# Optimization experiments

Hardware: AMD Instinct MI355X
Metric: run time of the kernel (lower is better)

## Reference

```python
import jax, jax.numpy as jnp
import numpy as np

IN_SHAPE, OUT_SHAPE = 64, 256  # FoldingBlock(64, 256, ...)
REPEAT = OUT_SHAPE // IN_SHAPE  # 4


def sample_2d(m, n):
    # Reproduces SANet.points + SANet.sample_2D exactly (numpy constants).
    xs = np.linspace(-0.3, 0.3, 46)
    ys = np.linspace(-0.3, 0.3, 46)
    X, Y = np.meshgrid(xs, ys)            # (46,46) each, 'xy' indexing
    pts = np.stack([X, Y])                # (2,46,46)
    ix = np.round(np.linspace(0, 45, m)).astype(int)
    iy = np.round(np.linspace(0, 45, n)).astype(int)
    gx, gy = np.meshgrid(ix, iy)          # (n,m)
    p = pts[:, gx.ravel(), gy.ravel()].T  # (m*n, 2)
    return jnp.asarray(p, dtype=jnp.float32)


def _lin_relu(x, W, b):
    return jax.nn.relu(x @ W + b)


def setup_inputs() -> dict:
    key = jax.random.key(0)
    ks = jax.random.split(key, 16)
    s = 0.02  # small init scale keeps softmax logits well-conditioned
    d = {
        "p": jax.random.normal(ks[0], (128, 64, 512), dtype=jnp.float32),
        # upmlp1: MLP([514, 512]) (shared by both up() calls)
        "W_up": jax.random.normal(ks[1], (514, 512), dtype=jnp.float32) * s,
        "b_up": jnp.zeros((512,), jnp.float32),
        # self_attn1: M_h = MLP([1024,256])
        "Wh": jax.random.normal(ks[2], (1024, 256), dtype=jnp.float32) * s,
        "bh": jnp.zeros((256,), jnp.float32),
        # M_l = MLP([1024,256])
        "Wl": jax.random.normal(ks[3], (1024, 256), dtype=jnp.float32) * s,
        "bl": jnp.zeros((256,), jnp.float32),
        # M_g = MLP([1024,1024])
        "Wg": jax.random.normal(ks[4], (1024, 1024), dtype=jnp.float32) * s,
        "bg": jnp.zeros((1024,), jnp.float32),
        # M_f = MLP([1024,512,256]) -> two Linear+ReLU layers
        "Wf1": jax.random.normal(ks[5], (1024, 512), dtype=jnp.float32) * s,
        "bf1": jnp.zeros((512,), jnp.float32),
        "Wf2": jax.random.normal(ks[6], (512, 256), dtype=jnp.float32) * s,
        "bf2": jnp.zeros((256,), jnp.float32),
        # M_down: MLP([1024, 512])
        "W_down": jax.random.normal(ks[7], (1024, 512), dtype=jnp.float32) * s,
        "b_down": jnp.zeros((512,), jnp.float32),
        "m": 16,
        "n": 16,
    }
    return d


def _up(p, pts, W_up, b_up, Wh, bh, Wl, bl, Wg, bg, Wf1, bf1, Wf2, bf2):
    # p: (B, 64, 512) -> (B, 256, 512) via torch-style repeat (tile)
    B = p.shape[0]
    p = jnp.tile(p, (1, REPEAT, 1))
    p2d = jnp.concatenate([p, jnp.broadcast_to(pts[None], (B,) + pts.shape)], -1)  # (B,256,514)
    p2d = _lin_relu(p2d, W_up, b_up)                  # (B,256,512)
    p = jnp.concatenate([p, p2d], -1)                  # (B,256,1024)
    # SelfAttention (hand-rolled: separate projections + softmax + bmm)
    h = _lin_relu(p, Wh, bh)                           # (B,256,256)
    l = _lin_relu(p, Wl, bl)                           # (B,256,256)
    g = _lin_relu(p, Wg, bg)                           # (B,256,1024)
    mm = jnp.einsum("bmc,bnc->bmn", l, h)             # l @ h^T
    attn = jax.nn.softmax(mm, axis=-1)
    applied = jnp.einsum("bmn,bnc->bmc", attn, g)      # (B,256,1024)
    x = p + applied
    # M_f = MLP([1024,512,256]): ReLU after every Linear
    return _lin_relu(_lin_relu(x, Wf1, bf1), Wf2, bf2)  # (B,256,256)


def _down(p, W_down, b_down):
    # (B,256,256) -> (B,64,1024) -> MLP([1024,512])
    B = p.shape[0]
    p = p.reshape(B, IN_SHAPE, REPEAT * p.shape[2])
    return _lin_relu(p, W_down, b_down)                # (B,64,512)


def reference(p, W_up, b_up, Wh, bh, Wl, bl, Wg, bg, Wf1, bf1, Wf2, bf2,
              W_down, b_down, m, n):
    pts = sample_2d(int(m), int(n))                    # (m*n, 2) constant grid
    attn_params = (Wh, bh, Wl, bl, Wg, bg, Wf1, bf1, Wf2, bf2)
    p1 = _up(p, pts, W_up, b_up, *attn_params)         # (B,256,256)
    p2 = _down(p1, W_down, b_down)                     # (B,64,512)
    p_delta = p - p2
    p2u = _up(p_delta, pts, W_up, b_up, *attn_params)  # shared weights with first up
    return p1 + p2u                                    # (B,256,256)
```

## Files before the change

kernel.cpp:

```cpp
#include <hip/hip_runtime.h>
#include <cstdint>
#include <cstddef>


typedef unsigned short u16;
typedef __bf16 bf16x8 __attribute__((ext_vector_type(8)));
typedef float f32x4 __attribute__((ext_vector_type(4)));

__device__ __forceinline__ u16 f2bf(float f) {
    unsigned u = __builtin_bit_cast(unsigned, f);
    unsigned r = (u + 0x7fffu + ((u >> 16) & 1u)) >> 16;
    return (u16)r;
}
__device__ __forceinline__ float bf2f(u16 h) {
    unsigned u = ((unsigned)h) << 16;
    return __builtin_bit_cast(float, u);
}
__device__ __forceinline__ bf16x8 ldfrag(const u16* p) {
    return __builtin_bit_cast(bf16x8, *reinterpret_cast<const uint4*>(p));
}
__device__ __forceinline__ void gload16(const u16* g, u16* l) {
    __builtin_amdgcn_global_load_lds((__attribute__((address_space(1))) void*)g,
                                     (__attribute__((address_space(3))) void*)l,
                                     16, 0, 0);
}

template<bool BIG, int MODE>
__global__ __launch_bounds__(BIG ? 512 : 256, 2)
void mg(const u16* __restrict__ A0, const u16* __restrict__ A1,
        const u16* __restrict__ Bt, const float* __restrict__ bias,
        const float* __restrict__ EXf,
        float* __restrict__ outF, u16* __restrict__ outB,
        u16* __restrict__ out1, u16* __restrict__ out2,
        int K, long sB)
{
    constexpr int BM = BIG ? 256 : 128;
    constexpr int BN = BIG ? 256 : 128;
    constexpr int BK = BIG ? 32 : 64;
    constexpr int THREADS = BIG ? 512 : 256;
    constexpr int WN = BIG ? 4 : 2;
    constexpr int MI = BIG ? 8 : 4;
    constexpr int NJ = 4;
    constexpr int KS = BK / 32;
    constexpr int UPR = BK / 8;
    constexpr int UMASK = UPR - 1;
    constexpr int USH = BIG ? 2 : 3;
    constexpr int RA = (BM * UPR) / THREADS;
    constexpr int RB = (BN * UPR) / THREADS;

    __shared__ __align__(16) u16 As[2][BM * BK];
    __shared__ __align__(16) u16 Bs[2][BN * BK];

    const int b    = blockIdx.z;
    const int tid  = threadIdx.x;
    const int lane = tid & 63;
    const int w    = tid >> 6;
    const int wr   = w / WN, wc = w % WN;
    const int wrow0 = wr * (BM / (THREADS / 64 / WN));
    const int wcol0 = wc * (BN / WN);
    const int gm0  = blockIdx.y * BM;
    const int gn0  = blockIdx.x * BN;
    const int lm   = lane & 15, hk = lane >> 4;

    const int NT = K / BK;

    auto stage = [&](int kt, int buf) {
        const int kb = kt * BK;
        #pragma unroll
        for (int t = 0; t < RA; ++t) {
            const int idx = tid + t * THREADS;
            const int row = idx >> USH, u = idx & UMASK;
            const int kk = kb + ((u ^ (row & UMASK)) << 3);
            const u16* ga;
            if constexpr (MODE == 0) {
                ga = A0 + ((size_t)b << 15) + (size_t)((gm0 + row) & 63) * 512 + kk;
            } else if constexpr (MODE == 1) {
                const int gr = gm0 + row;
                ga = (kk < 512) ? A0 + ((size_t)b << 15) + (size_t)(gr & 63) * 512 + kk
                                : A1 + ((size_t)b << 17) + (size_t)gr * 512 + (kk - 512);
            } else if constexpr (MODE == 2 || MODE == 3) {
                ga = A0 + ((size_t)b << 16) + (size_t)(gm0 + row) * 256 + kk;
            } else if constexpr (MODE == 4) {
                ga = A0 + ((size_t)b << 18) + (size_t)(gm0 + row) * 1024 + kk;
            } else if constexpr (MODE == 5) {
                ga = A0 + ((size_t)b << 17) + (size_t)(gm0 + row) * 512 + kk;
            } else {
                int gr = gm0 + row; if (gr > 63) gr = 63;
                ga = A0 + ((size_t)b << 16) + (size_t)(gr * 4 + (kk >> 8)) * 256 + (kk & 255);
            }
            gload16(ga, &As[buf][(size_t)(w * 64 + t * THREADS) * 8]);
        }
        #pragma unroll
        for (int t = 0; t < RB; ++t) {
            const int idx = tid + t * THREADS;
            const int row = idx >> USH, u = idx & UMASK;
            const int kk = kb + ((u ^ (row & UMASK)) << 3);
            gload16(Bt + (size_t)b * sB + (size_t)(gn0 + row) * K + kk,
                    &Bs[buf][(size_t)(w * 64 + t * THREADS) * 8]);
        }
    };

    f32x4 acc[MI][NJ];
    #pragma unroll
    for (int i = 0; i < MI; ++i)
        #pragma unroll
        for (int j = 0; j < NJ; ++j)
            acc[i][j] = (f32x4){0.f, 0.f, 0.f, 0.f};

    stage(0, 0);
    stage(1, 1);

    for (int kt = 0; kt < NT; ++kt) {
        const int cur = kt & 1;
        if (kt == NT - 1) {
            asm volatile("s_waitcnt vmcnt(0)" ::: "memory");
        } else if constexpr (RA + RB == 4) {
            asm volatile("s_waitcnt vmcnt(4)" ::: "memory");
        } else {
            asm volatile("s_waitcnt vmcnt(8)" ::: "memory");
        }
        __builtin_amdgcn_s_barrier();
        asm volatile("" ::: "memory");

        #pragma unroll
        for (int ks = 0; ks < KS; ++ks) {
            bf16x8 af[MI], bfr[NJ];
            #pragma unroll
            for (int i = 0; i < MI; ++i) {
                const int row = wrow0 + i * 16 + lm;
                af[i] = ldfrag(&As[cur][(size_t)row * BK + (((ks * 4 + hk) ^ (row & UMASK)) << 3)]);
            }
            #pragma unroll
            for (int j = 0; j < NJ; ++j) {
                const int row = wcol0 + j * 16 + lm;
                bfr[j] = ldfrag(&Bs[cur][(size_t)row * BK + (((ks * 4 + hk) ^ (row & UMASK)) << 3)]);
            }
            __builtin_amdgcn_s_setprio(1);
            #pragma unroll
            for (int i = 0; i < MI; ++i)
                #pragma unroll
                for (int j = 0; j < NJ; ++j)
                    acc[i][j] = __builtin_amdgcn_mfma_f32_16x16x32_bf16(af[i], bfr[j], acc[i][j], 0, 0, 0);
            __builtin_amdgcn_s_setprio(0);
        }

        asm volatile("" ::: "memory");
        __builtin_amdgcn_s_barrier();
        if (kt + 2 < NT) stage(kt + 2, cur);
    }

    #pragma unroll
    for (int i = 0; i < MI; ++i) {
        #pragma unroll
        for (int r = 0; r < 4; ++r) {
            const int row = gm0 + wrow0 + i * 16 + hk * 4 + r;
            if (MODE == 6 && row >= 64) continue;
            #pragma unroll
            for (int j = 0; j < NJ; ++j) {
                const int col = gn0 + wcol0 + j * 16 + lm;
                float v = acc[i][j][r];
                if constexpr (MODE == 0) {
                    const float px = -0.3f + 0.04f * (float)(row >> 4);
                    const float py = -0.3f + 0.04f * (float)(row & 15);
                    v += px * EXf[(size_t)512 * 512 + col] + py * EXf[(size_t)513 * 512 + col];
                    v = fmaxf(v + bias[col], 0.0f);
                    outB[((size_t)b << 17) + (size_t)row * 512 + col] = f2bf(v);
                } else if constexpr (MODE == 1) {
                    v = fmaxf(v + bias[col], 0.0f);
                    if (col < 256)      outB[((size_t)b << 16) + (size_t)row * 256 + col] = f2bf(v);
                    else if (col < 512) out1[((size_t)b << 16) + (size_t)row * 256 + (col - 256)] = f2bf(v);
                    else                out2[((size_t)b << 18) + (size_t)row * 1024 + (col - 512)] = f2bf(v);
                } else if constexpr (MODE == 2) {
                    outF[((size_t)b << 16) + (size_t)row * 256 + col] = v;
                } else if constexpr (MODE == 3) {
                    float cv = (col < 512)
                        ? EXf[((size_t)b << 15) + (size_t)(row & 63) * 512 + col]
                        : bf2f(A1[((size_t)b << 17) + (size_t)row * 512 + (col - 512)]);
                    v += cv;
                    outB[((size_t)b << 18) + (size_t)row * 1024 + col] = f2bf(v);
                } else if constexpr (MODE == 4) {
                    v = fmaxf(v + bias[col], 0.0f);
                    outB[((size_t)b << 17) + (size_t)row * 512 + col] = f2bf(v);
                } else if constexpr (MODE == 5) {
                    v = fmaxf(v + bias[col], 0.0f);
                    const size_t oidx = ((size_t)b << 16) + (size_t)row * 256 + col;
                    if (EXf) v += EXf[oidx];
                    outF[oidx] = v;
                    if (outB) outB[oidx] = f2bf(v);
                } else if constexpr (MODE == 6) {
                    v = fmaxf(v + bias[col], 0.0f);
                    const size_t oidx = ((size_t)b << 15) + (size_t)row * 512 + col;
                    v = EXf[oidx] - v;
                    outF[oidx] = v;
                    outB[oidx] = f2bf(v);
                }
            }
        }
    }
}

template<bool F32IN>
__global__ __launch_bounds__(256)
void transpose_k(const void* __restrict__ in_, u16* __restrict__ out, int R, int C)
{
    __shared__ float t[64][65];
    const size_t zo = (size_t)blockIdx.z * (size_t)R * C;
    const int c0 = blockIdx.x * 64, r0 = blockIdx.y * 64;
    const int x = threadIdx.x, y = threadIdx.y;
    #pragma unroll
    for (int i = 0; i < 16; ++i) {
        const int r = y * 16 + i;
        float v;
        if constexpr (F32IN) v = ((const float*)in_)[zo + (size_t)(r0 + r) * C + c0 + x];
        else                 v = bf2f(((const u16*)in_)[zo + (size_t)(r0 + r) * C + c0 + x]);
        t[r][x] = v;
    }
    __syncthreads();
    #pragma unroll
    for (int i = 0; i < 16; ++i) {
        const int c = y * 16 + i;
        out[zo + (size_t)(c0 + c) * R + r0 + x] = f2bf(t[x][c]);
    }
}

__global__ __launch_bounds__(256)
void cvt_k(const float* __restrict__ in, u16* __restrict__ out, int n4)
{
    int i = blockIdx.x * 256 + threadIdx.x;
    const int stride = gridDim.x * 256;
    for (; i < n4; i += stride) {
        float4 v = ((const float4*)in)[i];
        ushort4 o;
        o.x = f2bf(v.x); o.y = f2bf(v.y); o.z = f2bf(v.z); o.w = f2bf(v.w);
        ((ushort4*)out)[i] = o;
    }
}

__global__ __launch_bounds__(512)
void concat3_k(const float* __restrict__ a, const float* __restrict__ bb,
               const float* __restrict__ c, float* __restrict__ o)
{
    const int i = blockIdx.x * 512 + threadIdx.x;
    if (i < 256)       o[i] = a[i];
    else if (i < 512)  o[i] = bb[i - 256];
    else if (i < 1536) o[i] = c[i - 512];
}

__global__ __launch_bounds__(64)
void softmax_k(const float* __restrict__ logits, u16* __restrict__ attn)
{
    const size_t row = blockIdx.x;
    const float4 v = ((const float4*)(logits + row * 256))[threadIdx.x];
    float mx = fmaxf(fmaxf(v.x, v.y), fmaxf(v.z, v.w));
    #pragma unroll
    for (int o = 32; o > 0; o >>= 1) mx = fmaxf(mx, __shfl_xor(mx, o));
    float e0 = expf(v.x - mx), e1 = expf(v.y - mx), e2 = expf(v.z - mx), e3 = expf(v.w - mx);
    float s = e0 + e1 + e2 + e3;
    #pragma unroll
    for (int o = 32; o > 0; o >>= 1) s += __shfl_xor(s, o);
    const float inv = 1.0f / s;
    ushort4 o;
    o.x = f2bf(e0 * inv); o.y = f2bf(e1 * inv); o.z = f2bf(e2 * inv); o.w = f2bf(e3 * inv);
    ((ushort4*)(attn + row * 256))[threadIdx.x] = o;
}

extern "C" void kernel_launch(void* const* d_in, const int* in_sizes, int n_in,
                              void* d_out, int out_size, void* d_ws, size_t ws_size,
                              hipStream_t stream)
{
    const float* p      = (const float*)d_in[0];
    const float* W_up   = (const float*)d_in[1];
    const float* b_up   = (const float*)d_in[2];
    const float* Wh     = (const float*)d_in[3];
    const float* bh     = (const float*)d_in[4];
    const float* Wl     = (const float*)d_in[5];
    const float* bl     = (const float*)d_in[6];
    const float* Wg     = (const float*)d_in[7];
    const float* bg     = (const float*)d_in[8];
    const float* Wf1    = (const float*)d_in[9];
    const float* bf1    = (const float*)d_in[10];
    const float* Wf2    = (const float*)d_in[11];
    const float* bf2v   = (const float*)d_in[12];
    const float* W_down = (const float*)d_in[13];
    const float* b_down = (const float*)d_in[14];

    const int B = in_sizes[0] / 32768;
    float* out = (float*)d_out;

    char* wsp = (char*)d_ws;
    auto alloc = [&](size_t bytes) -> char* {
        char* r = wsp; wsp += (bytes + 255) & ~(size_t)255; return r;
    };

    u16* WupT  = (u16*)alloc((size_t)512 * 512 * 2);
    u16* WhlgT = (u16*)alloc((size_t)1536 * 1024 * 2);
    u16* Wf1T  = (u16*)alloc((size_t)512 * 1024 * 2);
    u16* Wf2T  = (u16*)alloc((size_t)256 * 512 * 2);
    u16* WdT   = (u16*)alloc((size_t)512 * 1024 * 2);
    float* bias_hlg = (float*)alloc((size_t)1536 * 4);
    u16* pbf   = (u16*)alloc((size_t)B * 32768 * 2);

    const size_t fixed_used = (size_t)(wsp - (char*)d_ws);
    const size_t perB = 2555904;
    int BC = B;
    while (BC > 1 && fixed_used + (size_t)BC * perB > ws_size) BC >>= 1;

    u16* upout = (u16*)alloc((size_t)BC * 131072 * 2);
    u16* gb    = (u16*)alloc((size_t)BC * 262144 * 2);
    u16* gT    = (u16*)alloc((size_t)BC * 262144 * 2);
    u16* xb    = gb;
    u16* hb    = (u16*)alloc((size_t)BC * 65536 * 2);
    u16* lb    = (u16*)alloc((size_t)BC * 65536 * 2);
    u16* atb   = (u16*)alloc((size_t)BC * 65536 * 2);
    u16* p1bf  = (u16*)alloc((size_t)BC * 65536 * 2);
    u16* pdbf  = (u16*)alloc((size_t)BC * 32768 * 2);
    float* lgt = (float*)alloc((size_t)BC * 65536 * 4);
    float* p1f = (float*)alloc((size_t)BC * 65536 * 4);
    float* pdf = (float*)alloc((size_t)BC * 32768 * 4);

    const dim3 tb(64, 4);
    {
        int n4 = B * 8192;
        int nb = (n4 + 255) / 256; if (nb > 2048) nb = 2048;
        cvt_k<<<dim3(nb), dim3(256), 0, stream>>>(p, pbf, n4);
        transpose_k<true><<<dim3(8, 8, 1),  tb, 0, stream>>>(W_up, WupT, 512, 512);
        transpose_k<true><<<dim3(4, 16, 1), tb, 0, stream>>>(Wh, WhlgT, 1024, 256);
        transpose_k<true><<<dim3(4, 16, 1), tb, 0, stream>>>(Wl, WhlgT + (size_t)256 * 1024, 1024, 256);
        transpose_k<true><<<dim3(16, 16, 1),tb, 0, stream>>>(Wg, WhlgT + (size_t)512 * 1024, 1024, 1024);
        transpose_k<true><<<dim3(8, 16, 1), tb, 0, stream>>>(Wf1, Wf1T, 1024, 512);
        transpose_k<true><<<dim3(4, 8, 1),  tb, 0, stream>>>(Wf2, Wf2T, 512, 256);
        transpose_k<true><<<dim3(8, 16, 1), tb, 0, stream>>>(W_down, WdT, 1024, 512);
        concat3_k<<<dim3(3), dim3(512), 0, stream>>>(bh, bl, bg, bias_hlg);
    }

    auto run_up = [&](const u16* pin_bf, const float* pin_f32,
                      float* f2outF, u16* f2outB, const float* f2EXf, int bc) {
        mg<false,0><<<dim3(4, 2, bc), dim3(256), 0, stream>>>(
            pin_bf, nullptr, WupT, b_up, W_up, nullptr, upout, nullptr, nullptr, 512, 0);
        mg<true,1><<<dim3(6, 1, bc), dim3(512), 0, stream>>>(
            pin_bf, upout, WhlgT, bias_hlg, nullptr, nullptr, hb, lb, gb, 1024, 0);
        mg<false,2><<<dim3(2, 2, bc), dim3(256), 0, stream>>>(
            lb, nullptr, hb, nullptr, nullptr, lgt, nullptr, nullptr, nullptr, 256, 65536);
        softmax_k<<<dim3(bc * 256), dim3(64), 0, stream>>>(lgt, atb);
        transpose_k<false><<<dim3(16, 4, bc), tb, 0, stream>>>(gb, gT, 256, 1024);
        mg<true,3><<<dim3(4, 1, bc), dim3(512), 0, stream>>>(
            atb, upout, gT, nullptr, pin_f32, nullptr, xb, nullptr, nullptr, 256, 262144);
        mg<false,4><<<dim3(4, 2, bc), dim3(256), 0, stream>>>(
            xb, nullptr, Wf1T, bf1, nullptr, nullptr, upout, nullptr, nullptr, 1024, 0);
        mg<false,5><<<dim3(2, 2, bc), dim3(256), 0, stream>>>(
            upout, nullptr, Wf2T, bf2v, f2EXf, f2outF, f2outB, nullptr, nullptr, 512, 0);
    };

    for (int b0 = 0; b0 < B; b0 += BC) {
        const int bc = (B - b0 < BC) ? (B - b0) : BC;
        const u16*   pin_bf  = pbf + (size_t)b0 * 32768;
        const float* pin_f32 = p   + (size_t)b0 * 32768;
        run_up(pin_bf, pin_f32, p1f, p1bf, nullptr, bc);
        mg<false,6><<<dim3(4, 1, bc), dim3(256), 0, stream>>>(
            p1bf, nullptr, WdT, b_down, pin_f32, pdf, pdbf, nullptr, nullptr, 1024, 0);
        run_up(pdbf, pdf, out + (size_t)b0 * 65536, nullptr, p1f, bc);
    }
}
```

Measured before the change: 1.023 ms.

## Split GEMM kernel into 256-tile 4-stage pipelined variant and fuse g transpose

Adds a dedicated 512-thread 256x256-tile GEMM kernel with a four-slot LDS ring (prefetch three tiles ahead, issued before the MFMAs) and a k-major unswizzled LDS layout. It is used for the up, hlg, attention-apply and f1 stages, while the small-tile kernel stays for logits, f2 and down. The hlg kernel now writes the g output already transposed, which removes the separate transpose launch. The down stage no longer writes an fp32 delta, and the second up pass reads the bf16 delta instead. The logits buffer is aliased onto xb to shrink the workspace, at the cost of 128KB LDS per block, which lowers occupancy, and of some precision in the residual.

```diff
diff --git a/kernel.cpp b/kernel.cpp
--- a/kernel.cpp
+++ b/kernel.cpp
@@ -25,121 +25,255 @@
                                      16, 0, 0);
 }
 
-template<bool BIG, int MODE>
-__global__ __launch_bounds__(BIG ? 512 : 256, 2)
-void mg(const u16* __restrict__ A0, const u16* __restrict__ A1,
+template<int MODE>
+__global__ __launch_bounds__(512, 2)
+void bg(const u16* __restrict__ A0, const u16* __restrict__ A1,
         const u16* __restrict__ Bt, const float* __restrict__ bias,
-        const float* __restrict__ EXf,
-        float* __restrict__ outF, u16* __restrict__ outB,
-        u16* __restrict__ out1, u16* __restrict__ out2,
+        const float* __restrict__ EXf, const u16* __restrict__ EXb,
+        u16* __restrict__ outB, u16* __restrict__ out1, u16* __restrict__ out2,
         int K, long sB)
 {
-    constexpr int BM = BIG ? 256 : 128;
-    constexpr int BN = BIG ? 256 : 128;
-    constexpr int BK = BIG ? 32 : 64;
-    constexpr int THREADS = BIG ? 512 : 256;
-    constexpr int WN = BIG ? 4 : 2;
-    constexpr int MI = BIG ? 8 : 4;
-    constexpr int NJ = 4;
-    constexpr int KS = BK / 32;
-    constexpr int UPR = BK / 8;
-    constexpr int UMASK = UPR - 1;
-    constexpr int USH = BIG ? 2 : 3;
-    constexpr int RA = (BM * UPR) / THREADS;
-    constexpr int RB = (BN * UPR) / THREADS;
-
-    __shared__ __align__(16) u16 As[2][BM * BK];
-    __shared__ __align__(16) u16 Bs[2][BN * BK];
+    __shared__ __align__(16) u16 As[4][256 * 32];
+    __shared__ __align__(16) u16 Bs[4][256 * 32];
 
     const int b    = blockIdx.z;
     const int tid  = threadIdx.x;
     const int lane = tid & 63;
     const int w    = tid >> 6;
-    const int wr   = w / WN, wc = w % WN;
-    const int wrow0 = wr * (BM / (THREADS / 64 / WN));
-    const int wcol0 = wc * (BN / WN);
-    const int gm0  = blockIdx.y * BM;
-    const int gn0  = blockIdx.x * BN;
+    const int wr   = w >> 2;
+    const int wc   = w & 3;
+    const int wrow0 = wr * 128;
+    const int wcol0 = wc * 64;
+    const int gn0  = blockIdx.x * 256;
     const int lm   = lane & 15, hk = lane >> 4;
 
+    const int NT = K / 32;
+
+    auto stage = [&](int kt, int slot) {
+        const int kb = kt * 32;
+        #pragma unroll
+        for (int t = 0; t < 2; ++t) {
+            const int idx = tid + t * 512;
+            const int U   = idx >> 8;
+            const int row = idx & 255;
+            const int k   = kb + U * 8;
+            const u16* ga;
+            if constexpr (MODE == 0) {
+                ga = A0 + ((size_t)b << 15) + (size_t)(row & 63) * 512 + k;
+            } else if constexpr (MODE == 1) {
+                ga = (k < 512) ? A0 + ((size_t)b << 15) + (size_t)(row & 63) * 512 + k
+                               : A1 + ((size_t)b << 17) + (size_t)row * 512 + (k - 512);
+            } else if constexpr (MODE == 3) {
+                ga = A0 + ((size_t)b << 16) + (size_t)row * 256 + k;
+            } else {
+                ga = A0 + ((size_t)b << 18) + (size_t)row * 1024 + k;
+            }
+            gload16(ga, &As[slot][(size_t)(t * 512 + w * 64) * 8]);
+        }
+        #pragma unroll
+        for (int t = 0; t < 2; ++t) {
+            const int idx = tid + t * 512;
+            const int U   = idx >> 8;
+            const int row = idx & 255;
+            const int k   = kb + U * 8;
+            gload16(Bt + (size_t)b * sB + (size_t)(gn0 + row) * K + k,
+                    &Bs[slot][(size_t)(t * 512 + w * 64) * 8]);
+        }
+    };
+
+    f32x4 acc[8][4];
+    #pragma unroll
+    for (int i = 0; i < 8; ++i)
+        #pragma unroll
+        for (int j = 0; j < 4; ++j)
+            acc[i][j] = (f32x4){0.f, 0.f, 0.f, 0.f};
+
+    stage(0, 0);
+    stage(1, 1);
+    stage(2, 2);
+
+    for (int kt = 0; kt < NT; ++kt) {
+        const int s = kt & 3;
+        const int rem = NT - 1 - kt;
+        if (rem >= 2)      asm volatile("s_waitcnt vmcnt(8)" ::: "memory");
+        else if (rem == 1) asm volatile("s_waitcnt vmcnt(4)" ::: "memory");
+        else               asm volatile("s_waitcnt vmcnt(0)" ::: "memory");
+        __builtin_amdgcn_s_barrier();
+        asm volatile("" ::: "memory");
+
+        bf16x8 af[8], bfr[4];
+        #pragma unroll
+        for (int i = 0; i < 8; ++i)
+            af[i] = ldfrag(&As[s][(size_t)hk * 2048 + (size_t)(wrow0 + i * 16 + lm) * 8]);
+        #pragma unroll
+        for (int j = 0; j < 4; ++j)
+            bfr[j] = ldfrag(&Bs[s][(size_t)hk * 2048 + (size_t)(wcol0 + j * 16 + lm) * 8]);
+
+        if (kt + 3 < NT) stage(kt + 3, (kt + 3) & 3);
+
+        __builtin_amdgcn_s_setprio(1);
+        #pragma unroll
+        for (int i = 0; i < 8; ++i)
+            #pragma unroll
+            for (int j = 0; j < 4; ++j)
+                acc[i][j] = __builtin_amdgcn_mfma_f32_16x16x32_bf16(af[i], bfr[j], acc[i][j], 0, 0, 0);
+        __builtin_amdgcn_s_setprio(0);
+        asm volatile("" ::: "memory");
+    }
+
+    #pragma unroll
+    for (int i = 0; i < 8; ++i) {
+        const int rowb = wrow0 + i * 16 + hk * 4;
+        #pragma unroll
+        for (int j = 0; j < 4; ++j) {
+            const int col = gn0 + wcol0 + j * 16 + lm;
+            float v4[4];
+            #pragma unroll
+            for (int r = 0; r < 4; ++r) v4[r] = acc[i][j][r];
+
+            if constexpr (MODE == 0) {
+                #pragma unroll
+                for (int r = 0; r < 4; ++r) {
+                    const int row = rowb + r;
+                    float v = v4[r];
+                    const float px = -0.3f + 0.04f * (float)(row >> 4);
+                    const float py = -0.3f + 0.04f * (float)(row & 15);
+                    v += px * EXf[(size_t)512 * 512 + col] + py * EXf[(size_t)513 * 512 + col];
+                    v = fmaxf(v + bias[col], 0.0f);
+                    outB[((size_t)b << 17) + (size_t)row * 512 + col] = f2bf(v);
+                }
+            } else if constexpr (MODE == 1) {
+                if (col < 512) {
+                    #pragma unroll
+                    for (int r = 0; r < 4; ++r) {
+                        const int row = rowb + r;
+                        float v = fmaxf(v4[r] + bias[col], 0.0f);
+                        if (col < 256) outB[((size_t)b << 16) + (size_t)row * 256 + col] = f2bf(v);
+                        else           out1[((size_t)b << 16) + (size_t)row * 256 + (col - 256)] = f2bf(v);
+                    }
+                } else {
+                    ushort4 o;
+                    o.x = f2bf(fmaxf(v4[0] + bias[col], 0.0f));
+                    o.y = f2bf(fmaxf(v4[1] + bias[col], 0.0f));
+                    o.z = f2bf(fmaxf(v4[2] + bias[col], 0.0f));
+                    o.w = f2bf(fmaxf(v4[3] + bias[col], 0.0f));
+                    *reinterpret_cast<ushort4*>(out2 + ((size_t)b << 18) +
+                        (size_t)(col - 512) * 256 + rowb) = o;
+                }
+            } else if constexpr (MODE == 3) {
+                #pragma unroll
+                for (int r = 0; r < 4; ++r) {
+                    const int row = rowb + r;
+                    float v = v4[r];
+                    float cv;
+                    if (col < 512) {
+                        const size_t ridx = ((size_t)b << 15) + (size_t)(row & 63) * 512 + col;
+                        cv = EXf ? EXf[ridx] : bf2f(EXb[ridx]);
+                    } else {
+                        cv = bf2f(A1[((size_t)b << 17) + (size_t)row * 512 + (col - 512)]);
+                    }
+                    v += cv;
+                    outB[((size_t)b << 18) + (size_t)row * 1024 + col] = f2bf(v);
+                }
+            } else {
+                #pragma unroll
+                for (int r = 0; r < 4; ++r) {
+                    const int row = rowb + r;
+                    float v = fmaxf(v4[r] + bias[col], 0.0f);
+                    outB[((size_t)b << 17) + (size_t)row * 512 + col] = f2bf(v);
+                }
+            }
+        }
+    }
+}
+
+template<int MODE>
+__global__ __launch_bounds__(256, 2)
+void mg(const u16* __restrict__ A0, const u16* __restrict__ Bt,
+        const float* __restrict__ bias, const float* __restrict__ EXf,
+        float* __restrict__ outF, u16* __restrict__ outB,
+        int K, long sB)
+{
+    constexpr int BK = 64;
+    constexpr int UMASK = 7;
+
+    __shared__ __align__(16) u16 As[2][128 * 64];
+    __shared__ __align__(16) u16 Bs[2][128 * 64];
+
+    const int b    = blockIdx.z;
+    const int tid  = threadIdx.x;
+    const int lane = tid & 63;
+    const int w    = tid >> 6;
+    const int wr   = w >> 1, wc = w & 1;
+    const int wrow0 = wr * 64, wcol0 = wc * 64;
+    const int gm0  = blockIdx.y * 128;
+    const int gn0  = blockIdx.x * 128;
+    const int lm   = lane & 15, hk = lane >> 4;
     const int NT = K / BK;
 
     auto stage = [&](int kt, int buf) {
         const int kb = kt * BK;
         #pragma unroll
-        for (int t = 0; t < RA; ++t) {
-            const int idx = tid + t * THREADS;
-            const int row = idx >> USH, u = idx & UMASK;
+        for (int t = 0; t < 4; ++t) {
+            const int idx = tid + t * 256;
+            const int row = idx >> 3, u = idx & UMASK;
             const int kk = kb + ((u ^ (row & UMASK)) << 3);
             const u16* ga;
-            if constexpr (MODE == 0) {
-                ga = A0 + ((size_t)b << 15) + (size_t)((gm0 + row) & 63) * 512 + kk;
-            } else if constexpr (MODE == 1) {
-                const int gr = gm0 + row;
-                ga = (kk < 512) ? A0 + ((size_t)b << 15) + (size_t)(gr & 63) * 512 + kk
-                                : A1 + ((size_t)b << 17) + (size_t)gr * 512 + (kk - 512);
-            } else if constexpr (MODE == 2 || MODE == 3) {
+            if constexpr (MODE == 2) {
                 ga = A0 + ((size_t)b << 16) + (size_t)(gm0 + row) * 256 + kk;
-            } else if constexpr (MODE == 4) {
-                ga = A0 + ((size_t)b << 18) + (size_t)(gm0 + row) * 1024 + kk;
             } else if constexpr (MODE == 5) {
                 ga = A0 + ((size_t)b << 17) + (size_t)(gm0 + row) * 512 + kk;
             } else {
                 int gr = gm0 + row; if (gr > 63) gr = 63;
                 ga = A0 + ((size_t)b << 16) + (size_t)(gr * 4 + (kk >> 8)) * 256 + (kk & 255);
             }
-            gload16(ga, &As[buf][(size_t)(w * 64 + t * THREADS) * 8]);
-        }
-        #pragma unroll
-        for (int t = 0; t < RB; ++t) {
-            const int idx = tid + t * THREADS;
-            const int row = idx >> USH, u = idx & UMASK;
+            gload16(ga, &As[buf][(size_t)(w * 64 + t * 256) * 8]);
+        }
+        #pragma unroll
+        for (int t = 0; t < 4; ++t) {
+            const int idx = tid + t * 256;
+            const int row = idx >> 3, u = idx & UMASK;
             const int kk = kb + ((u ^ (row & UMASK)) << 3);
             gload16(Bt + (size_t)b * sB + (size_t)(gn0 + row) * K + kk,
-                    &Bs[buf][(size_t)(w * 64 + t * THREADS) * 8]);
+                    &Bs[buf][(size_t)(w * 64 + t * 256) * 8]);
         }
     };
 
-    f32x4 acc[MI][NJ];
-    #pragma unroll
-    for (int i = 0; i < MI; ++i)
-        #pragma unroll
-        for (int j = 0; j < NJ; ++j)
+    f32x4 acc[4][4];
+    #pragma unroll
+    for (int i = 0; i < 4; ++i)
+        #pragma unroll
+        for (int j = 0; j < 4; ++j)
             acc[i][j] = (f32x4){0.f, 0.f, 0.f, 0.f};
 
     stage(0, 0);
-    stage(1, 1);
+    if (NT > 1) stage(1, 1);
 
     for (int kt = 0; kt < NT; ++kt) {
         const int cur = kt & 1;
-        if (kt == NT - 1) {
-            asm volatile("s_waitcnt vmcnt(0)" ::: "memory");
-        } else if constexpr (RA + RB == 4) {
-            asm volatile("s_waitcnt vmcnt(4)" ::: "memory");
-        } else {
-            asm volatile("s_waitcnt vmcnt(8)" ::: "memory");
-        }
+        if (kt == NT - 1) asm volatile("s_waitcnt vmcnt(0)" ::: "memory");
+        else              asm volatile("s_waitcnt vmcnt(8)" ::: "memory");
         __builtin_amdgcn_s_barrier();
         asm volatile("" ::: "memory");
 
         #pragma unroll
-        for (int ks = 0; ks < KS; ++ks) {
-            bf16x8 af[MI], bfr[NJ];
-            #pragma unroll
-            for (int i = 0; i < MI; ++i) {
+        for (int ks = 0; ks < 2; ++ks) {
+            bf16x8 af[4], bfr[4];
+            #pragma unroll
+            for (int i = 0; i < 4; ++i) {
                 const int row = wrow0 + i * 16 + lm;
                 af[i] = ldfrag(&As[cur][(size_t)row * BK + (((ks * 4 + hk) ^ (row & UMASK)) << 3)]);
             }
             #pragma unroll
-            for (int j = 0; j < NJ; ++j) {
+            for (int j = 0; j < 4; ++j) {
                 const int row = wcol0 + j * 16 + lm;
                 bfr[j] = ldfrag(&Bs[cur][(size_t)row * BK + (((ks * 4 + hk) ^ (row & UMASK)) << 3)]);
             }
             __builtin_amdgcn_s_setprio(1);
             #pragma unroll
-            for (int i = 0; i < MI; ++i)
+            for (int i = 0; i < 4; ++i)
                 #pragma unroll
-                for (int j = 0; j < NJ; ++j)
+                for (int j = 0; j < 4; ++j)
                     acc[i][j] = __builtin_amdgcn_mfma_f32_16x16x32_bf16(af[i], bfr[j], acc[i][j], 0, 0, 0);
             __builtin_amdgcn_s_setprio(0);
         }
@@ -150,48 +284,27 @@
     }
 
     #pragma unroll
-    for (int i = 0; i < MI; ++i) {
+    for (int i = 0; i < 4; ++i) {
         #pragma unroll
         for (int r = 0; r < 4; ++r) {
             const int row = gm0 + wrow0 + i * 16 + hk * 4 + r;
             if (MODE == 6 && row >= 64) continue;
             #pragma unroll
-            for (int j = 0; j < NJ; ++j) {
+            for (int j = 0; j < 4; ++j) {
                 const int col = gn0 + wcol0 + j * 16 + lm;
                 float v = acc[i][j][r];
-                if constexpr (MODE == 0) {
-                    const float px = -0.3f + 0.04f * (float)(row >> 4);
-                    const float py = -0.3f + 0.04f * (float)(row & 15);
-                    v += px * EXf[(size_t)512 * 512 + col] + py * EXf[(size_t)513 * 512 + col];
-                    v = fmaxf(v + bias[col], 0.0f);
-                    outB[((size_t)b << 17) + (size_t)row * 512 + col] = f2bf(v);
-                } else if constexpr (MODE == 1) {
-                    v = fmaxf(v + bias[col], 0.0f);
-                    if (col < 256)      outB[((size_t)b << 16) + (size_t)row * 256 + col] = f2bf(v);
-                    else if (col < 512) out1[((size_t)b << 16) + (size_t)row * 256 + (col - 256)] = f2bf(v);
-                    else                out2[((size_t)b << 18) + (size_t)row * 1024 + (col - 512)] = f2bf(v);
-                } else if constexpr (MODE == 2) {
+                if constexpr (MODE == 2) {
                     outF[((size_t)b << 16) + (size_t)row * 256 + col] = v;
-                } else if constexpr (MODE == 3) {
-                    float cv = (col < 512)
-                        ? EXf[((size_t)b << 15) + (size_t)(row & 63) * 512 + col]
-                        : bf2f(A1[((size_t)b << 17) + (size_t)row * 512 + (col - 512)]);
-                    v += cv;
-                    outB[((size_t)b << 18) + (size_t)row * 1024 + col] = f2bf(v);
-                } else if constexpr (MODE == 4) {
-                    v = fmaxf(v + bias[col], 0.0f);
-                    outB[((size_t)b << 17) + (size_t)row * 512 + col] = f2bf(v);
                 } else if constexpr (MODE == 5) {
                     v = fmaxf(v + bias[col], 0.0f);
                     const size_t oidx = ((size_t)b << 16) + (size_t)row * 256 + col;
                     if (EXf) v += EXf[oidx];
                     outF[oidx] = v;
                     if (outB) outB[oidx] = f2bf(v);
-                } else if constexpr (MODE == 6) {
+                } else {
                     v = fmaxf(v + bias[col], 0.0f);
                     const size_t oidx = ((size_t)b << 15) + (size_t)row * 512 + col;
                     v = EXf[oidx] - v;
-                    outF[oidx] = v;
                     outB[oidx] = f2bf(v);
                 }
             }
@@ -276,7 +389,7 @@
     const float* Wl     = (const float*)d_in[5];
     const float* bl     = (const float*)d_in[6];
     const float* Wg     = (const float*)d_in[7];
-    const float* bg     = (const float*)d_in[8];
+    const float* bg_    = (const float*)d_in[8];
     const float* Wf1    = (const float*)d_in[9];
     const float* bf1    = (const float*)d_in[10];
     const float* Wf2    = (const float*)d_in[11];
@@ -301,22 +414,20 @@
     u16* pbf   = (u16*)alloc((size_t)B * 32768 * 2);
 
     const size_t fixed_used = (size_t)(wsp - (char*)d_ws);
-    const size_t perB = 2555904;
+    const size_t perB = 2162688;
     int BC = B;
-    while (BC > 1 && fixed_used + (size_t)BC * perB > ws_size) BC >>= 1;
+    while (BC > 1 && fixed_used + (size_t)BC * perB + 4096 > ws_size) BC >>= 1;
 
     u16* upout = (u16*)alloc((size_t)BC * 131072 * 2);
-    u16* gb    = (u16*)alloc((size_t)BC * 262144 * 2);
     u16* gT    = (u16*)alloc((size_t)BC * 262144 * 2);
-    u16* xb    = gb;
+    u16* xb    = (u16*)alloc((size_t)BC * 262144 * 2);
     u16* hb    = (u16*)alloc((size_t)BC * 65536 * 2);
     u16* lb    = (u16*)alloc((size_t)BC * 65536 * 2);
     u16* atb   = (u16*)alloc((size_t)BC * 65536 * 2);
     u16* p1bf  = (u16*)alloc((size_t)BC * 65536 * 2);
     u16* pdbf  = (u16*)alloc((size_t)BC * 32768 * 2);
-    float* lgt = (float*)alloc((size_t)BC * 65536 * 4);
     float* p1f = (float*)alloc((size_t)BC * 65536 * 4);
-    float* pdf = (float*)alloc((size_t)BC * 32768 * 4);
+    float* lgt = (float*)xb;
 
     const dim3 tb(64, 4);
     {
@@ -330,34 +441,33 @@
         transpose_k<true><<<dim3(8, 16, 1), tb, 0, stream>>>(Wf1, Wf1T, 1024, 512);
         transpose_k<true><<<dim3(4, 8, 1),  tb, 0, stream>>>(Wf2, Wf2T, 512, 256);
         transpose_k<true><<<dim3(8, 16, 1), tb, 0, stream>>>(W_down, WdT, 1024, 512);
-        concat3_k<<<dim3(3), dim3(512), 0, stream>>>(bh, bl, bg, bias_hlg);
-    }
-
-    auto run_up = [&](const u16* pin_bf, const float* pin_f32,
+        concat3_k<<<dim3(3), dim3(512), 0, stream>>>(bh, bl, bg_, bias_hlg);
+    }
+
+    auto run_up = [&](const u16* pin_bf, const float* pin_f32, const u16* pin_ebf,
                       float* f2outF, u16* f2outB, const float* f2EXf, int bc) {
-        mg<false,0><<<dim3(4, 2, bc), dim3(256), 0, stream>>>(
+        bg<0><<<dim3(2, 1, bc), dim3(512), 0, stream>>>(
             pin_bf, nullptr, WupT, b_up, W_up, nullptr, upout, nullptr, nullptr, 512, 0);
-        mg<true,1><<<dim3(6, 1, bc), dim3(512), 0, stream>>>(
-            pin_bf, upout, WhlgT, bias_hlg, nullptr, nullptr, hb, lb, gb, 1024, 0);
-        mg<false,2><<<dim3(2, 2, bc), dim3(256), 0, stream>>>(
-            lb, nullptr, hb, nullptr, nullptr, lgt, nullptr, nullptr, nullptr, 256, 65536);
+        bg<1><<<dim3(6, 1, bc), dim3(512), 0, stream>>>(
+            pin_bf, upout, WhlgT, bias_hlg, nullptr, nullptr, hb, lb, gT, 1024, 0);
+        mg<2><<<dim3(2, 2, bc), dim3(256), 0, stream>>>(
+            lb, hb, nullptr, nullptr, lgt, nullptr, 256, 65536);
         softmax_k<<<dim3(bc * 256), dim3(64), 0, stream>>>(lgt, atb);
-        transpose_k<false><<<dim3(16, 4, bc), tb, 0, stream>>>(gb, gT, 256, 1024);
-        mg<true,3><<<dim3(4, 1, bc), dim3(512), 0, stream>>>(
-            atb, upout, gT, nullptr, pin_f32, nullptr, xb, nullptr, nullptr, 256, 262144);
-        mg<false,4><<<dim3(4, 2, bc), dim3(256), 0, stream>>>(
+        bg<3><<<dim3(4, 1, bc), dim3(512), 0, stream>>>(
+            atb, upout, gT, nullptr, pin_f32, pin_ebf, xb, nullptr, nullptr, 256, 262144);
+        bg<4><<<dim3(2, 1, bc), dim3(512), 0, stream>>>(
             xb, nullptr, Wf1T, bf1, nullptr, nullptr, upout, nullptr, nullptr, 1024, 0);
-        mg<false,5><<<dim3(2, 2, bc), dim3(256), 0, stream>>>(
-            upout, nullptr, Wf2T, bf2v, f2EXf, f2outF, f2outB, nullptr, nullptr, 512, 0);
+        mg<5><<<dim3(2, 2, bc), dim3(256), 0, stream>>>(
+            upout, Wf2T, bf2v, f2EXf, f2outF, f2outB, 512, 0);
     };
 
     for (int b0 = 0; b0 < B; b0 += BC) {
         const int bc = (B - b0 < BC) ? (B - b0) : BC;
         const u16*   pin_bf  = pbf + (size_t)b0 * 32768;
         const float* pin_f32 = p   + (size_t)b0 * 32768;
-        run_up(pin_bf, pin_f32, p1f, p1bf, nullptr, bc);
-        mg<false,6><<<dim3(4, 1, bc), dim3(256), 0, stream>>>(
-            p1bf, nullptr, WdT, b_down, pin_f32, pdf, pdbf, nullptr, nullptr, 1024, 0);
-        run_up(pdbf, pdf, out + (size_t)b0 * 65536, nullptr, p1f, bc);
-    }
-}
+        run_up(pin_bf, pin_f32, nullptr, p1f, p1bf, nullptr, bc);
+        mg<6><<<dim3(4, 1, bc), dim3(256), 0, stream>>>(
+            p1bf, WdT, b_down, pin_f32, nullptr, pdbf, 1024, 0);
+        run_up(pdbf, nullptr, pdbf, out + (size_t)b0 * 65536, nullptr, p1f, bc);
+    }
+}
```

After: 1.095 ms. 7.0% more time.
